# Optimization experiments

Hardware: AMD Instinct MI355X
Metric: run time of the kernel (lower is better)

The kernel has to match this reference:

```python
import jax, jax.numpy as jnp
import numpy as np

VOCAB, EMB, HID = 120000, 64, 128
B, T = 256, 512


def _rnn_layer(inp, W_ih, b_ih, W_hh, b_hh):
    # inp: [B,T,D]. PyTorch RNN: h_t = tanh(W_ih x_t + b_ih + W_hh h_{t-1} + b_hh)
    pre = jnp.einsum('btd,hd->bth', inp, W_ih) + b_ih + b_hh  # input part hoisted out of scan
    h0 = jnp.zeros((inp.shape[0], W_hh.shape[0]), inp.dtype)

    def step(h, p_t):
        h = jnp.tanh(p_t + h @ W_hh.T)
        return h, h

    hT, outs = jax.lax.scan(step, h0, pre.transpose(1, 0, 2))  # scan over time
    return outs.transpose(1, 0, 2), hT  # [B,T,H], [B,H]


def _layernorm(x, g, b, eps=1e-5):
    mu = jnp.mean(x, axis=-1, keepdims=True)
    var = jnp.var(x, axis=-1, keepdims=True)
    return (x - mu) * jax.lax.rsqrt(var + eps) * g + b


def setup_inputs() -> dict:
    key = jax.random.key(0)
    ks = jax.random.split(key, 10)
    emb = jax.random.normal(ks[0], (VOCAB, EMB), jnp.float32) * 0.02
    emb = emb.at[0].set(0.0)  # padding_idx=0
    s_in, s_h = 1.0 / np.sqrt(HID), 1.0 / np.sqrt(HID)
    return {
        'x': jax.random.randint(ks[1], (B, T), 0, VOCAB),
        'emb': emb,
        'W_ih1': jax.random.normal(ks[2], (HID, EMB), jnp.float32) * s_in,
        'b_ih1': jnp.zeros((HID,), jnp.float32),
        'W_hh1': jax.random.normal(ks[3], (HID, HID), jnp.float32) * s_h,
        'b_hh1': jnp.zeros((HID,), jnp.float32),
        'W_ih2': jax.random.normal(ks[4], (HID, HID), jnp.float32) * s_in,
        'b_ih2': jnp.zeros((HID,), jnp.float32),
        'W_hh2': jax.random.normal(ks[5], (HID, HID), jnp.float32) * s_h,
        'b_hh2': jnp.zeros((HID,), jnp.float32),
        'ln_g': jnp.ones((HID,), jnp.float32),
        'ln_b': jnp.zeros((HID,), jnp.float32),
        'proj_W': jax.random.normal(ks[6], (HID, HID), jnp.float32) * s_h,
        'proj_b': jnp.zeros((HID,), jnp.float32),
        'on_g': jnp.ones((HID,), jnp.float32),
        'on_b': jnp.zeros((HID,), jnp.float32),
    }


def reference(x, emb, W_ih1, b_ih1, W_hh1, b_hh1, W_ih2, b_ih2, W_hh2, b_hh2,
              ln_g, ln_b, proj_W, proj_b, on_g, on_b):
    e = emb[x]                                   # [B,T,64]
    out1, _ = _rnn_layer(e, W_ih1, b_ih1, W_hh1, b_hh1)   # dropout is identity in eval
    _, h2 = _rnn_layer(out1, W_ih2, b_ih2, W_hh2, b_hh2)  # h2: [B,128] (last hidden state)
    rep = _layernorm(h2, ln_g, ln_b)
    rep = jnp.tanh(rep @ proj_W.T + proj_b)
    rep = _layernorm(rep, on_g, on_b)
    return rep
```

## Files before the change

kernel.cpp:

```cpp
#include <hip/hip_runtime.h>

#define BT (256*512)
#define HID 128
#define EMB 64
#define CH 32

__device__ __forceinline__ float fast_tanh(float x) {
    float e = __expf(2.f * x);
    return 1.f - __fdividef(2.f, e + 1.f);
}

#define OPQ(v) asm volatile("" : "+v"(v.x), "+v"(v.y), "+v"(v.z), "+v"(v.w))

#define DPPADD(v, ctrl) ((v) + __int_as_float(__builtin_amdgcn_mov_dpp(__float_as_int(v), (ctrl), 0xF, 0xF, false)))

#define RACC(P, Q, wa, wb, wc, wd) \
    P = fmaf(hv0.x, wa.x, P); Q = fmaf(hv0.y, wa.y, Q); \
    P = fmaf(hv0.z, wa.z, P); Q = fmaf(hv0.w, wa.w, Q); \
    P = fmaf(hv1.x, wb.x, P); Q = fmaf(hv1.y, wb.y, Q); \
    P = fmaf(hv1.z, wb.z, P); Q = fmaf(hv1.w, wb.w, Q); \
    P = fmaf(hv2.x, wc.x, P); Q = fmaf(hv2.y, wc.y, Q); \
    P = fmaf(hv2.z, wc.z, P); Q = fmaf(hv2.w, wc.w, Q); \
    P = fmaf(hv3.x, wd.x, P); Q = fmaf(hv3.y, wd.y, Q); \
    P = fmaf(hv3.z, wd.z, P); Q = fmaf(hv3.w, wd.w, Q);

__global__ __launch_bounds__(256)
__attribute__((amdgpu_waves_per_eu(1, 2)))
void k_embed_pre1(
    const int* __restrict__ x, const float* __restrict__ emb,
    const float* __restrict__ Wih1, const float* __restrict__ bih1,
    const float* __restrict__ bhh1, float* __restrict__ pre1)
{
    __shared__ float sA[32][128];
    __shared__ float sW[32][132];
    __shared__ int stok[128];
    const int tid = threadIdx.x;
    const int base = blockIdx.x * 128;
    const int tx = tid & 15, ty = tid >> 4;
    const int ox = tx * 8, py = ty * 8;
    const int pl = tid & 127, half = tid >> 7;
    if (tid < 128) stok[tid] = x[base + tid];
    float acc[8][8];
#pragma unroll
    for (int p = 0; p < 8; ++p)
#pragma unroll
        for (int o = 0; o < 8; ++o) acc[p][o] = 0.f;
    __syncthreads();
    const float4* ws = (const float4*)(Wih1 + (size_t)pl * EMB + half * 16);
    const float4* as = (const float4*)(emb + (size_t)stok[pl] * EMB + half * 16);
    float4 qw[2][4], qe[2][4];
#pragma unroll
    for (int kc = 0; kc < 2; ++kc)
#pragma unroll
        for (int k = 0; k < 4; ++k) {
            qw[kc][k] = ws[kc * 8 + k];
            qe[kc][k] = as[kc * 8 + k];
        }
    for (int kc = 0; kc < 2; ++kc) {
        {
            const int jb = half * 16;
#pragma unroll
            for (int k = 0; k < 4; ++k) {
                float4 q = qw[kc][k], e = qe[kc][k];
                sW[jb + 4*k + 0][pl] = q.x; sW[jb + 4*k + 1][pl] = q.y;
                sW[jb + 4*k + 2][pl] = q.z; sW[jb + 4*k + 3][pl] = q.w;
                sA[jb + 4*k + 0][pl] = e.x; sA[jb + 4*k + 1][pl] = e.y;
                sA[jb + 4*k + 2][pl] = e.z; sA[jb + 4*k + 3][pl] = e.w;
            }
        }
        __syncthreads();
#pragma unroll 4
        for (int j = 0; j < 32; ++j) {
            float4 a0 = *(const float4*)&sA[j][py];
            float4 a1 = *(const float4*)&sA[j][py + 4];
            float4 b0 = *(const float4*)&sW[j][ox];
            float4 b1 = *(const float4*)&sW[j][ox + 4];
            float av[8] = {a0.x,a0.y,a0.z,a0.w,a1.x,a1.y,a1.z,a1.w};
            float bv[8] = {b0.x,b0.y,b0.z,b0.w,b1.x,b1.y,b1.z,b1.w};
#pragma unroll
            for (int p = 0; p < 8; ++p)
#pragma unroll
                for (int o = 0; o < 8; ++o)
                    acc[p][o] = fmaf(av[p], bv[o], acc[p][o]);
        }
        __syncthreads();
    }
    float bo[8];
#pragma unroll
    for (int o = 0; o < 8; ++o) bo[o] = bih1[ox + o] + bhh1[ox + o];
#pragma unroll
    for (int p = 0; p < 8; ++p) {
        float* cp = pre1 + (size_t)(base + py + p) * HID + ox;
        *(float4*)cp       = make_float4(acc[p][0]+bo[0], acc[p][1]+bo[1], acc[p][2]+bo[2], acc[p][3]+bo[3]);
        *(float4*)(cp + 4) = make_float4(acc[p][4]+bo[4], acc[p][5]+bo[5], acc[p][6]+bo[6], acc[p][7]+bo[7]);
    }
}

__device__ inline float bsum768(float v, volatile float* sc, int tid) {
#pragma unroll
    for (int off = 32; off > 0; off >>= 1) v += __shfl_down(v, off, 64);
    __syncthreads();
    if ((tid & 63) == 0) sc[tid >> 6] = v;
    __syncthreads();
    float s = 0.f;
#pragma unroll
    for (int k = 0; k < 12; ++k) s += sc[k];
    return s;
}

__global__ __launch_bounds__(768)
__attribute__((amdgpu_waves_per_eu(1, 3)))
void k_rnn_fused(
    const float* __restrict__ pre1, const float* __restrict__ Whh1,
    const float* __restrict__ Wih2, const float* __restrict__ bih2,
    const float* __restrict__ bhh2, const float* __restrict__ Whh2,
    const float* __restrict__ ln_g, const float* __restrict__ ln_b,
    const float* __restrict__ projW, const float* __restrict__ proj_b,
    const float* __restrict__ on_g, const float* __restrict__ on_b,
    float* __restrict__ out)
{
    __shared__ __align__(16) float h1[2][160];
    __shared__ __align__(16) float h2[2][160];
    __shared__ __align__(16) float spre[CH * HID];
    __shared__ float sfin[HID];
    __shared__ float sc[12];

    const int bb   = blockIdx.x;
    const int tid  = threadIdx.x;
    const int w    = tid >> 6;
    const int lane = tid & 63;
    const bool L1  = (w < 4);
    const int  e   = lane & 7;
    const int  m   = L1 ? 0 : ((lane >> 3) & 1);
    const int  rg  = L1 ? (lane >> 3) : (lane >> 4);
    const int  rowbase = L1 ? (32 * w + rg) : (16 * (w - 4) + rg);
    const int  rstep   = L1 ? 8 : 4;
    const float* wmat  = L1 ? Whh1 : (m ? Whh2 : Wih2);

    const float4* wr0 = (const float4*)(wmat + (size_t)(rowbase            ) * HID + e * 16);
    const float4* wr1 = (const float4*)(wmat + (size_t)(rowbase +     rstep) * HID + e * 16);
    const float4* wr2 = (const float4*)(wmat + (size_t)(rowbase + 2 * rstep) * HID + e * 16);
    const float4* wr3 = (const float4*)(wmat + (size_t)(rowbase + 3 * rstep) * HID + e * 16);
    float4 w0 = wr0[0], w1 = wr0[1], w2  = wr0[2], w3  = wr0[3],
           w4 = wr1[0], w5 = wr1[1], w6  = wr1[2], w7  = wr1[3],
           w8 = wr2[0], w9 = wr2[1], w10 = wr2[2], w11 = wr2[3],
           w12= wr3[0], w13= wr3[1], w14 = wr3[2], w15 = wr3[3];
    OPQ(w0);OPQ(w1);OPQ(w2);OPQ(w3);OPQ(w4);OPQ(w5);OPQ(w6);OPQ(w7);
    OPQ(w8);OPQ(w9);OPQ(w10);OPQ(w11);OPQ(w12);OPQ(w13);OPQ(w14);OPQ(w15);

    const bool wr_en = L1 ? (e < 4) : (m == 0 && e < 4);
    const int  wrow  = rowbase + (e & 3) * rstep;
    const int  wword = ((wrow >> 4) * 20) + (wrow & 15);
    const float b2w  = (!L1 && wr_en) ? (bih2[wrow] + bhh2[wrow]) : 0.f;

    if (tid < 160) { h1[0][tid] = 0.f; h2[0][tid] = 0.f; }

    const float* srcb = (L1 || m == 0) ? &h1[0][0] : &h2[0][0];
    const float4* rp0 = (const float4*)(srcb + e * 20);
    const float4* rp1 = (const float4*)(srcb + 160 + e * 20);
    float* dstb = L1 ? &h1[0][0] : &h2[0][0];
    float* wp_e = dstb + 160 + wword;
    float* wp_o = dstb + wword;

    const float4* gsrc = (const float4*)(pre1 + (size_t)bb * 512 * HID);
    float4* spv = (float4*)spre;
    float4 pf0, pf1;
    if (tid < 512) { pf0 = gsrc[tid]; pf1 = gsrc[tid + 512]; }
    __syncthreads();

    auto do_step = [&](int t, int s, const float4* rp, float* wpt) {
        float4 hv0 = rp[0], hv1 = rp[1], hv2 = rp[2], hv3 = rp[3];
        float p0=0,q0=0,p1=0,q1=0,p2=0,q2=0,p3=0,q3=0;
        RACC(p0,q0, w0,w1,w2,w3)
        RACC(p1,q1, w4,w5,w6,w7)
        RACC(p2,q2, w8,w9,w10,w11)
        RACC(p3,q3, w12,w13,w14,w15)
        float s0 = p0+q0, s1 = p1+q1, s2 = p2+q2, s3 = p3+q3;
        s0 = DPPADD(s0, 0xB1); s1 = DPPADD(s1, 0xB1); s2 = DPPADD(s2, 0xB1); s3 = DPPADD(s3, 0xB1);
        s0 = DPPADD(s0, 0x4E); s1 = DPPADD(s1, 0x4E); s2 = DPPADD(s2, 0x4E); s3 = DPPADD(s3, 0x4E);
        s0 = DPPADD(s0, 0x141); s1 = DPPADD(s1, 0x141); s2 = DPPADD(s2, 0x141); s3 = DPPADD(s3, 0x141);
        if (!L1) {
            s0 = DPPADD(s0, 0x140); s1 = DPPADD(s1, 0x140);
            s2 = DPPADD(s2, 0x140); s3 = DPPADD(s3, 0x140);
        }
        if (wr_en) {
            float ta = (e & 1) ? s1 : s0;
            float tb = (e & 1) ? s3 : s2;
            float v  = (e & 2) ? tb : ta;
            if (L1) *wpt = fast_tanh(spre[s * HID + wrow] + v);
            else    *wpt = (t > 0) ? fast_tanh(b2w + v) : 0.f;
        }
        __syncthreads();
    };

#pragma unroll 1
    for (int c = 0; c < 512 / CH; ++c) {
        if (tid < 512) { spv[tid] = pf0; spv[tid + 512] = pf1; }
        __syncthreads();
        if (c < 512 / CH - 1 && tid < 512) {
            pf0 = gsrc[(c + 1) * 1024 + tid];
            pf1 = gsrc[(c + 1) * 1024 + tid + 512];
        }
        const int t0 = c * CH;
#pragma unroll 1
        for (int s = 0; s < CH; s += 2) {
            do_step(t0 + s,     s,     rp0, wp_e);
            do_step(t0 + s + 1, s + 1, rp1, wp_o);
        }
    }

    {
        float* wpD = L1 ? wp_e : &sfin[wrow];
        do_step(512, 0, rp0, wpD);
    }

    const int i = tid & 127;
    float hn = (tid < 128) ? sfin[i] : 0.f;
    float s1v = bsum768(hn, sc, tid);
    float s2v = bsum768(hn * hn, sc, tid);
    float mu = s1v * (1.f / 128.f);
    float var = s2v * (1.f / 128.f) - mu * mu;
    __syncthreads();
    if (tid < 128) spre[i] = (hn - mu) * rsqrtf(var + 1e-5f) * ln_g[i] + ln_b[i];
    __syncthreads();
    float pv = 0.f;
    if (tid < 128) {
        float a0 = proj_b[i], a1 = 0, a2 = 0, a3 = 0;
        const float4* hp = (const float4*)spre;
        const float4* pr = (const float4*)(projW + (size_t)i * HID);
#pragma unroll
        for (int k = 0; k < HID / 4; ++k) {
            float4 u = pr[k];
            float4 hv = hp[k];
            a0 = fmaf(hv.x, u.x, a0); a1 = fmaf(hv.y, u.y, a1);
            a2 = fmaf(hv.z, u.z, a2); a3 = fmaf(hv.w, u.w, a3);
        }
        pv = tanhf((a0 + a1) + (a2 + a3));
    }
    float t1 = bsum768(pv, sc, tid);
    float t2 = bsum768(pv * pv, sc, tid);
    float mu2 = t1 * (1.f / 128.f);
    float var2 = t2 * (1.f / 128.f) - mu2 * mu2;
    if (tid < 128)
        out[(size_t)bb * HID + i] = (pv - mu2) * rsqrtf(var2 + 1e-5f) * on_g[i] + on_b[i];
}

extern "C" void kernel_launch(void* const* d_in, const int* in_sizes, int n_in,
                              void* d_out, int out_size, void* d_ws, size_t ws_size,
                              hipStream_t stream)
{
    const int*   x     = (const int*)  d_in[0];
    const float* emb   = (const float*)d_in[1];
    const float* Wih1  = (const float*)d_in[2];
    const float* bih1  = (const float*)d_in[3];
    const float* Whh1  = (const float*)d_in[4];
    const float* bhh1  = (const float*)d_in[5];
    const float* Wih2  = (const float*)d_in[6];
    const float* bih2  = (const float*)d_in[7];
    const float* Whh2  = (const float*)d_in[8];
    const float* bhh2  = (const float*)d_in[9];
    const float* ln_g  = (const float*)d_in[10];
    const float* ln_b  = (const float*)d_in[11];
    const float* projW = (const float*)d_in[12];
    const float* projb = (const float*)d_in[13];
    const float* on_g  = (const float*)d_in[14];
    const float* on_b  = (const float*)d_in[15];

    float* pre1 = (float*)d_ws;

    k_embed_pre1<<<BT / 128, 256, 0, stream>>>(x, emb, Wih1, bih1, bhh1, pre1);
    k_rnn_fused<<<256, 768, 0, stream>>>(pre1, Whh1, Wih2, bih2, bhh2, Whh2,
                                         ln_g, ln_b, projW, projb, on_g, on_b,
                                         (float*)d_out);
}
```

Measured before the change: 447.9 us.

## Restructure fused RNN to 512 threads with 6 rows per lane-group and pipelined layer-2 input projection

Reworks the fused two-layer recurrence kernel from 768 to 512 threads. Each 8-lane group now computes six 16-wide partial dot products, spread over 384 rows: Whh1, Wih2 and Whh2. The layer-2 input projection is staged through a double-buffered PP array one step behind, so each step needs only one dot product per row instead of a split two-matrix sum. The DPP reduction is written in inline asm, and the pre1 values are prefetched per thread from global memory rather than staged in shared-memory chunks. This cuts wave count and barrier cost per step, but adds one extra pipeline stage, more register pressure, and a global load on the critical path.

```diff
diff --git a/kernel.cpp b/kernel.cpp
--- a/kernel.cpp
+++ b/kernel.cpp
@@ -3,7 +3,6 @@
 #define BT (256*512)
 #define HID 128
 #define EMB 64
-#define CH 32
 
 __device__ __forceinline__ float fast_tanh(float x) {
     float e = __expf(2.f * x);
@@ -12,17 +11,24 @@
 
 #define OPQ(v) asm volatile("" : "+v"(v.x), "+v"(v.y), "+v"(v.z), "+v"(v.w))
 
-#define DPPADD(v, ctrl) ((v) + __int_as_float(__builtin_amdgcn_mov_dpp(__float_as_int(v), (ctrl), 0xF, 0xF, false)))
-
-#define RACC(P, Q, wa, wb, wc, wd) \
-    P = fmaf(hv0.x, wa.x, P); Q = fmaf(hv0.y, wa.y, Q); \
-    P = fmaf(hv0.z, wa.z, P); Q = fmaf(hv0.w, wa.w, Q); \
-    P = fmaf(hv1.x, wb.x, P); Q = fmaf(hv1.y, wb.y, Q); \
-    P = fmaf(hv1.z, wb.z, P); Q = fmaf(hv1.w, wb.w, Q); \
-    P = fmaf(hv2.x, wc.x, P); Q = fmaf(hv2.y, wc.y, Q); \
-    P = fmaf(hv2.z, wc.z, P); Q = fmaf(hv2.w, wc.w, Q); \
-    P = fmaf(hv3.x, wd.x, P); Q = fmaf(hv3.y, wd.y, Q); \
-    P = fmaf(hv3.z, wd.z, P); Q = fmaf(hv3.w, wd.w, Q);
+#define DOT16(d, A0, A1, A2, A3, WJ) \
+    d = A0.x*WJ[0].x; d = fmaf(A0.y, WJ[0].y, d); d = fmaf(A0.z, WJ[0].z, d); d = fmaf(A0.w, WJ[0].w, d); \
+    d = fmaf(A1.x, WJ[1].x, d); d = fmaf(A1.y, WJ[1].y, d); d = fmaf(A1.z, WJ[1].z, d); d = fmaf(A1.w, WJ[1].w, d); \
+    d = fmaf(A2.x, WJ[2].x, d); d = fmaf(A2.y, WJ[2].y, d); d = fmaf(A2.z, WJ[2].z, d); d = fmaf(A2.w, WJ[2].w, d); \
+    d = fmaf(A3.x, WJ[3].x, d); d = fmaf(A3.y, WJ[3].y, d); d = fmaf(A3.z, WJ[3].z, d); d = fmaf(A3.w, WJ[3].w, d);
+
+#define RSTG6(ctrl) \
+    "v_add_f32_dpp %0, %0, %0 " ctrl " row_mask:0xf bank_mask:0xf\n\t" \
+    "v_add_f32_dpp %1, %1, %1 " ctrl " row_mask:0xf bank_mask:0xf\n\t" \
+    "v_add_f32_dpp %2, %2, %2 " ctrl " row_mask:0xf bank_mask:0xf\n\t" \
+    "v_add_f32_dpp %3, %3, %3 " ctrl " row_mask:0xf bank_mask:0xf\n\t" \
+    "v_add_f32_dpp %4, %4, %4 " ctrl " row_mask:0xf bank_mask:0xf\n\t" \
+    "v_add_f32_dpp %5, %5, %5 " ctrl " row_mask:0xf bank_mask:0xf\n\t"
+#define REDUCE6 asm("s_nop 1\n\t" \
+    RSTG6("quad_perm:[1,0,3,2]") \
+    RSTG6("quad_perm:[2,3,0,1]") \
+    RSTG6("row_half_mirror") \
+    : "+v"(s0), "+v"(s1), "+v"(s2), "+v"(s3), "+v"(s4), "+v"(s5))
 
 __global__ __launch_bounds__(256)
 __attribute__((amdgpu_waves_per_eu(1, 2)))
@@ -96,7 +102,7 @@
     }
 }
 
-__device__ inline float bsum768(float v, volatile float* sc, int tid) {
+__device__ inline float bsum512(float v, volatile float* sc, int tid) {
 #pragma unroll
     for (int off = 32; off > 0; off >>= 1) v += __shfl_down(v, off, 64);
     __syncthreads();
@@ -104,12 +110,12 @@
     __syncthreads();
     float s = 0.f;
 #pragma unroll
-    for (int k = 0; k < 12; ++k) s += sc[k];
+    for (int k = 0; k < 8; ++k) s += sc[k];
     return s;
 }
 
-__global__ __launch_bounds__(768)
-__attribute__((amdgpu_waves_per_eu(1, 3)))
+__global__ __launch_bounds__(512)
+__attribute__((amdgpu_waves_per_eu(2)))
 void k_rnn_fused(
     const float* __restrict__ pre1, const float* __restrict__ Whh1,
     const float* __restrict__ Wih2, const float* __restrict__ bih2,
@@ -119,114 +125,127 @@
     const float* __restrict__ on_g, const float* __restrict__ on_b,
     float* __restrict__ out)
 {
-    __shared__ __align__(16) float h1[2][160];
-    __shared__ __align__(16) float h2[2][160];
-    __shared__ __align__(16) float spre[CH * HID];
+    __shared__ __align__(16) float H1[2][160];
+    __shared__ __align__(16) float H2[2][160];
+    __shared__ __align__(16) float PP[2][HID];
     __shared__ float sfin[HID];
-    __shared__ float sc[12];
+    __shared__ float xn[HID];
+    __shared__ float sc[8];
 
     const int bb   = blockIdx.x;
     const int tid  = threadIdx.x;
-    const int w    = tid >> 6;
-    const int lane = tid & 63;
-    const bool L1  = (w < 4);
-    const int  e   = lane & 7;
-    const int  m   = L1 ? 0 : ((lane >> 3) & 1);
-    const int  rg  = L1 ? (lane >> 3) : (lane >> 4);
-    const int  rowbase = L1 ? (32 * w + rg) : (16 * (w - 4) + rg);
-    const int  rstep   = L1 ? 8 : 4;
-    const float* wmat  = L1 ? Whh1 : (m ? Whh2 : Wih2);
-
-    const float4* wr0 = (const float4*)(wmat + (size_t)(rowbase            ) * HID + e * 16);
-    const float4* wr1 = (const float4*)(wmat + (size_t)(rowbase +     rstep) * HID + e * 16);
-    const float4* wr2 = (const float4*)(wmat + (size_t)(rowbase + 2 * rstep) * HID + e * 16);
-    const float4* wr3 = (const float4*)(wmat + (size_t)(rowbase + 3 * rstep) * HID + e * 16);
-    float4 w0 = wr0[0], w1 = wr0[1], w2  = wr0[2], w3  = wr0[3],
-           w4 = wr1[0], w5 = wr1[1], w6  = wr1[2], w7  = wr1[3],
-           w8 = wr2[0], w9 = wr2[1], w10 = wr2[2], w11 = wr2[3],
-           w12= wr3[0], w13= wr3[1], w14 = wr3[2], w15 = wr3[3];
-    OPQ(w0);OPQ(w1);OPQ(w2);OPQ(w3);OPQ(w4);OPQ(w5);OPQ(w6);OPQ(w7);
-    OPQ(w8);OPQ(w9);OPQ(w10);OPQ(w11);OPQ(w12);OPQ(w13);OPQ(w14);OPQ(w15);
-
-    const bool wr_en = L1 ? (e < 4) : (m == 0 && e < 4);
-    const int  wrow  = rowbase + (e & 3) * rstep;
-    const int  wword = ((wrow >> 4) * 20) + (wrow & 15);
-    const float b2w  = (!L1 && wr_en) ? (bih2[wrow] + bhh2[wrow]) : 0.f;
-
-    if (tid < 160) { h1[0][tid] = 0.f; h2[0][tid] = 0.f; }
-
-    const float* srcb = (L1 || m == 0) ? &h1[0][0] : &h2[0][0];
-    const float4* rp0 = (const float4*)(srcb + e * 20);
-    const float4* rp1 = (const float4*)(srcb + 160 + e * 20);
-    float* dstb = L1 ? &h1[0][0] : &h2[0][0];
-    float* wp_e = dstb + 160 + wword;
-    float* wp_o = dstb + wword;
-
-    const float4* gsrc = (const float4*)(pre1 + (size_t)bb * 512 * HID);
-    float4* spv = (float4*)spre;
-    float4 pf0, pf1;
-    if (tid < 512) { pf0 = gsrc[tid]; pf1 = gsrc[tid + 512]; }
-    __syncthreads();
-
-    auto do_step = [&](int t, int s, const float4* rp, float* wpt) {
-        float4 hv0 = rp[0], hv1 = rp[1], hv2 = rp[2], hv3 = rp[3];
-        float p0=0,q0=0,p1=0,q1=0,p2=0,q2=0,p3=0,q3=0;
-        RACC(p0,q0, w0,w1,w2,w3)
-        RACC(p1,q1, w4,w5,w6,w7)
-        RACC(p2,q2, w8,w9,w10,w11)
-        RACC(p3,q3, w12,w13,w14,w15)
-        float s0 = p0+q0, s1 = p1+q1, s2 = p2+q2, s3 = p3+q3;
-        s0 = DPPADD(s0, 0xB1); s1 = DPPADD(s1, 0xB1); s2 = DPPADD(s2, 0xB1); s3 = DPPADD(s3, 0xB1);
-        s0 = DPPADD(s0, 0x4E); s1 = DPPADD(s1, 0x4E); s2 = DPPADD(s2, 0x4E); s3 = DPPADD(s3, 0x4E);
-        s0 = DPPADD(s0, 0x141); s1 = DPPADD(s1, 0x141); s2 = DPPADD(s2, 0x141); s3 = DPPADD(s3, 0x141);
-        if (!L1) {
-            s0 = DPPADD(s0, 0x140); s1 = DPPADD(s1, 0x140);
-            s2 = DPPADD(s2, 0x140); s3 = DPPADD(s3, 0x140);
-        }
-        if (wr_en) {
-            float ta = (e & 1) ? s1 : s0;
-            float tb = (e & 1) ? s3 : s2;
-            float v  = (e & 2) ? tb : ta;
-            if (L1) *wpt = fast_tanh(spre[s * HID + wrow] + v);
-            else    *wpt = (t > 0) ? fast_tanh(b2w + v) : 0.f;
+    const int w    = tid >> 6, lane = tid & 63;
+    const int e    = lane & 7;
+    const int rg   = lane >> 3;
+    const int cls  = (w < 5) ? 0 : ((w == 5) ? 1 : 2);
+
+    float4 W4[6][4];
+#pragma unroll
+    for (int j = 0; j < 6; ++j) {
+        const int R = w * 48 + j * 8 + rg;
+        const float* wp = (R < 128) ? (Whh1 + (size_t)R * HID)
+                        : (R < 256) ? (Wih2 + (size_t)(R - 128) * HID)
+                                    : (Whh2 + (size_t)(R - 256) * HID);
+        const float4* wv = (const float4*)(wp + e * 16);
+#pragma unroll
+        for (int k = 0; k < 4; ++k) W4[j][k] = wv[k];
+    }
+#pragma unroll
+    for (int j = 0; j < 6; ++j) { OPQ(W4[j][0]); OPQ(W4[j][1]); OPQ(W4[j][2]); OPQ(W4[j][3]); }
+
+    const bool wr   = (e < 6);
+    const int  Rw   = w * 48 + e * 8 + rg;
+    const bool isH1 = wr && (Rw < 128);
+    const bool isP  = wr && (Rw >= 128) && (Rw < 256);
+    const bool isH2 = wr && (Rw >= 256);
+    float* wpE; float* wpO;
+    if (isH1)      { const int i0 = ((Rw >> 4) * 20) + (Rw & 15); wpE = &H1[1][i0]; wpO = &H1[0][i0]; }
+    else if (isP)  { const int i0 = Rw - 128;                     wpE = &PP[1][i0]; wpO = &PP[0][i0]; }
+    else if (isH2) { const int r2 = Rw - 256;
+                     const int i0 = ((r2 >> 4) * 20) + (r2 & 15); wpE = &H2[1][i0]; wpO = &H2[0][i0]; }
+    else           { wpE = &sc[0]; wpO = &sc[0]; }
+    const float b2w = isH2 ? (bih2[Rw - 256] + bhh2[Rw - 256]) : 0.f;
+    const float* prE = isH2 ? &PP[0][Rw - 256] : &PP[0][0];
+    const float* prO = isH2 ? &PP[1][Rw - 256] : &PP[1][0];
+
+    const float4* hpE = (const float4*)(&H1[0][e * 20]);
+    const float4* hpO = (const float4*)(&H1[1][e * 20]);
+    const float4* gpE = (const float4*)(&H2[0][e * 20]);
+    const float4* gpO = (const float4*)(&H2[1][e * 20]);
+
+    if (tid < 160) { H1[0][tid] = 0.f; H1[1][tid] = 0.f; H2[0][tid] = 0.f; H2[1][tid] = 0.f; }
+    if (tid < 128) { PP[0][tid] = 0.f; PP[1][tid] = 0.f; }
+
+    const float* preblk = pre1 + (size_t)bb * 512 * HID;
+    float pA = 0.f, pB = 0.f;
+    if (isH1) { pA = preblk[Rw]; pB = preblk[HID + Rw]; }
+    __syncthreads();
+
+    auto stepf = [&](const float4* hp, const float4* gp, const float* pr,
+                     float* wp, float& pslot, int tn, bool zeroH2, bool toSfin) {
+        const float pv = pslot;
+        float s0, s1, s2, s3, s4, s5;
+        if (cls == 0) {
+            float4 a0 = hp[0], a1 = hp[1], a2 = hp[2], a3 = hp[3];
+            DOT16(s0, a0,a1,a2,a3, W4[0]); DOT16(s1, a0,a1,a2,a3, W4[1]);
+            DOT16(s2, a0,a1,a2,a3, W4[2]); DOT16(s3, a0,a1,a2,a3, W4[3]);
+            DOT16(s4, a0,a1,a2,a3, W4[4]); DOT16(s5, a0,a1,a2,a3, W4[5]);
+        } else if (cls == 1) {
+            float4 a0 = hp[0], a1 = hp[1], a2 = hp[2], a3 = hp[3];
+            float4 g0 = gp[0], g1 = gp[1], g2 = gp[2], g3 = gp[3];
+            DOT16(s0, a0,a1,a2,a3, W4[0]); DOT16(s1, a0,a1,a2,a3, W4[1]);
+            DOT16(s2, g0,g1,g2,g3, W4[2]); DOT16(s3, g0,g1,g2,g3, W4[3]);
+            DOT16(s4, g0,g1,g2,g3, W4[4]); DOT16(s5, g0,g1,g2,g3, W4[5]);
+        } else {
+            float4 g0 = gp[0], g1 = gp[1], g2 = gp[2], g3 = gp[3];
+            DOT16(s0, g0,g1,g2,g3, W4[0]); DOT16(s1, g0,g1,g2,g3, W4[1]);
+            DOT16(s2, g0,g1,g2,g3, W4[2]); DOT16(s3, g0,g1,g2,g3, W4[3]);
+            DOT16(s4, g0,g1,g2,g3, W4[4]); DOT16(s5, g0,g1,g2,g3, W4[5]);
+        }
+        REDUCE6;
+        float ta = (e & 1) ? s1 : s0;
+        float tb = (e & 1) ? s3 : s2;
+        float tc = (e & 1) ? s5 : s4;
+        float u  = (e & 2) ? tb : ta;
+        float v  = (e & 4) ? tc : u;
+        float Prd = 0.f;
+        if (isH2) Prd = *pr;
+        const float add = isH1 ? pv : (isH2 ? (Prd + b2w) : 0.f);
+        const float vf  = v + add;
+        const float tv  = fast_tanh(vf);
+        float res = isP ? vf : tv;
+        if (zeroH2 && isH2) res = 0.f;
+        if (isH1) pslot = preblk[(size_t)tn * HID + Rw];
+        if (wr) {
+            if (toSfin) { if (isH2) sfin[Rw - 256] = res; }
+            else        *wp = res;
         }
         __syncthreads();
     };
 
+    stepf(hpE, gpE, prE, wpE, pA, 2, true, false);
+    stepf(hpO, gpO, prO, wpO, pB, 3, true, false);
 #pragma unroll 1
-    for (int c = 0; c < 512 / CH; ++c) {
-        if (tid < 512) { spv[tid] = pf0; spv[tid + 512] = pf1; }
-        __syncthreads();
-        if (c < 512 / CH - 1 && tid < 512) {
-            pf0 = gsrc[(c + 1) * 1024 + tid];
-            pf1 = gsrc[(c + 1) * 1024 + tid + 512];
-        }
-        const int t0 = c * CH;
-#pragma unroll 1
-        for (int s = 0; s < CH; s += 2) {
-            do_step(t0 + s,     s,     rp0, wp_e);
-            do_step(t0 + s + 1, s + 1, rp1, wp_o);
-        }
-    }
-
-    {
-        float* wpD = L1 ? wp_e : &sfin[wrow];
-        do_step(512, 0, rp0, wpD);
-    }
+    for (int t = 2; t < 512; t += 2) {
+        stepf(hpE, gpE, prE, wpE, pA, (t + 2 < 512) ? t + 2 : 511, false, false);
+        stepf(hpO, gpO, prO, wpO, pB, (t + 3 < 512) ? t + 3 : 511, false, false);
+    }
+    stepf(hpE, gpE, prE, wpE, pA, 511, false, false);
+    stepf(hpO, gpO, prO, wpO, pB, 511, false, true);
 
     const int i = tid & 127;
     float hn = (tid < 128) ? sfin[i] : 0.f;
-    float s1v = bsum768(hn, sc, tid);
-    float s2v = bsum768(hn * hn, sc, tid);
-    float mu = s1v * (1.f / 128.f);
+    float s1v = bsum512(hn, sc, tid);
+    float s2v = bsum512(hn * hn, sc, tid);
+    float mu  = s1v * (1.f / 128.f);
     float var = s2v * (1.f / 128.f) - mu * mu;
     __syncthreads();
-    if (tid < 128) spre[i] = (hn - mu) * rsqrtf(var + 1e-5f) * ln_g[i] + ln_b[i];
-    __syncthreads();
-    float pv = 0.f;
+    if (tid < 128) xn[i] = (hn - mu) * rsqrtf(var + 1e-5f) * ln_g[i] + ln_b[i];
+    __syncthreads();
+    float pvv = 0.f;
     if (tid < 128) {
         float a0 = proj_b[i], a1 = 0, a2 = 0, a3 = 0;
-        const float4* hp = (const float4*)spre;
+        const float4* hp = (const float4*)xn;
         const float4* pr = (const float4*)(projW + (size_t)i * HID);
 #pragma unroll
         for (int k = 0; k < HID / 4; ++k) {
@@ -235,14 +254,14 @@
             a0 = fmaf(hv.x, u.x, a0); a1 = fmaf(hv.y, u.y, a1);
             a2 = fmaf(hv.z, u.z, a2); a3 = fmaf(hv.w, u.w, a3);
         }
-        pv = tanhf((a0 + a1) + (a2 + a3));
-    }
-    float t1 = bsum768(pv, sc, tid);
-    float t2 = bsum768(pv * pv, sc, tid);
-    float mu2 = t1 * (1.f / 128.f);
+        pvv = tanhf((a0 + a1) + (a2 + a3));
+    }
+    float t1 = bsum512(pvv, sc, tid);
+    float t2 = bsum512(pvv * pvv, sc, tid);
+    float mu2  = t1 * (1.f / 128.f);
     float var2 = t2 * (1.f / 128.f) - mu2 * mu2;
     if (tid < 128)
-        out[(size_t)bb * HID + i] = (pv - mu2) * rsqrtf(var2 + 1e-5f) * on_g[i] + on_b[i];
+        out[(size_t)bb * HID + i] = (pvv - mu2) * rsqrtf(var2 + 1e-5f) * on_g[i] + on_b[i];
 }
 
 extern "C" void kernel_launch(void* const* d_in, const int* in_sizes, int n_in,
@@ -269,7 +288,7 @@
     float* pre1 = (float*)d_ws;
 
     k_embed_pre1<<<BT / 128, 256, 0, stream>>>(x, emb, Wih1, bih1, bhh1, pre1);
-    k_rnn_fused<<<256, 768, 0, stream>>>(pre1, Whh1, Wih2, bih2, bhh2, Whh2,
+    k_rnn_fused<<<256, 512, 0, stream>>>(pre1, Whh1, Wih2, bih2, bhh2, Whh2,
                                          ln_g, ln_b, projW, projb, on_g, on_b,
                                          (float*)d_out);
 }
```

Measured after the change: 471.2 us. 1.05x slower.
